# Optimization experiments

Measured on AMD Instinct MI355X. Metric: run time of the kernel, lower is better.

The kernel has to match this reference:

```python
import jax, jax.numpy as jnp
import numpy as np

B, N, D, H = 4, 4096, 1024, 16
DK = D // H  # 64


def setup_inputs() -> dict:
    key = jax.random.key(0)
    ks = jax.random.split(key, 11)
    s_in = 1.0 / np.sqrt(D)
    s_out = 1.0 / np.sqrt(H * DK)
    return {
        "query": jax.random.normal(ks[0], (B, N, D), jnp.float32),
        "key": jax.random.normal(ks[1], (B, N, D), jnp.float32),
        "value": jax.random.normal(ks[2], (B, N, D), jnp.float32),
        # stacked per-head Linear weights (torch Linear: y = x @ W.T + b)
        "Wq": jax.random.uniform(ks[3], (H, DK, D), jnp.float32, -s_in, s_in),
        "bq": jax.random.uniform(ks[4], (H, DK), jnp.float32, -s_in, s_in),
        "Wk": jax.random.uniform(ks[5], (H, DK, D), jnp.float32, -s_in, s_in),
        "bk": jax.random.uniform(ks[6], (H, DK), jnp.float32, -s_in, s_in),
        "Wv": jax.random.uniform(ks[7], (H, DK, D), jnp.float32, -s_in, s_in),
        "bv": jax.random.uniform(ks[8], (H, DK), jnp.float32, -s_in, s_in),
        "Wo": jax.random.uniform(ks[9], (D, H * DK), jnp.float32, -s_out, s_out),
        "bo": jax.random.uniform(ks[10], (D,), jnp.float32, -s_out, s_out),
    }


def reference(query, key, value, Wq, bq, Wk, bk, Wv, bv, Wo, bo):
    b, n, _ = query.shape
    # batched per-head projections: [b,h,n,d_k]
    q = jnp.einsum('bnd,hkd->bhnk', query, Wq) + bq[None, :, None, :]
    k = jnp.einsum('bnd,hkd->bhnk', key, Wk) + bk[None, :, None, :]
    v = jnp.einsum('bnd,hkd->bhnk', value, Wv) + bv[None, :, None, :]
    # linear dot-product attention (faithful: scale by batch**-0.5)
    q = jax.nn.softmax(q, axis=-1) * (b ** -0.5)
    k = jax.nn.softmax(k, axis=-2)  # softmax over sequence dim
    ctx = jnp.einsum('bhnd,bhne->bhde', k, v)      # [b,h,d_k,d_v]
    attn = jnp.einsum('bhnd,bhde->bhne', q, ctx)   # [b,h,n,d_v]
    # concat heads along last dim: [b,n,h*d_v]
    concat = attn.transpose(0, 2, 1, 3).reshape(b, n, -1)
    return concat @ Wo.T + bo
```

## Files before the change

kernel.cpp:

```cpp
#include <hip/hip_runtime.h>
#include <hip/hip_bf16.h>
#include <stdint.h>

#define B_  4
#define N_  4096
#define D_  1024
#define H_  16
#define DK_ 64
#define M_  (B_ * N_)

typedef __attribute__((ext_vector_type(8))) short  short8;
typedef __attribute__((ext_vector_type(4))) float  f32x4;
typedef __attribute__((ext_vector_type(4))) unsigned int u32x4;

__device__ __forceinline__ uint16_t f2bf(float f) {
  union { float f; uint32_t u; } v; v.f = f;
  uint32_t r = v.u + 0x7FFF + ((v.u >> 16) & 1);
  return (uint16_t)(r >> 16);
}
__device__ __forceinline__ uint32_t f2bf2(float lo, float hi) {
  return (uint32_t)f2bf(lo) | ((uint32_t)f2bf(hi) << 16);
}
__device__ __forceinline__ float bf2f(uint16_t u) {
  union { uint32_t u; float f; } v; v.u = ((uint32_t)u) << 16;
  return v.f;
}

__device__ __forceinline__ void gload_lds16(const void* g, void* l) {
  __builtin_amdgcn_global_load_lds((const __attribute__((address_space(1))) void*)g,
                                   (__attribute__((address_space(3))) void*)l, 16, 0, 0);
}

#define S_BARRIER() __builtin_amdgcn_s_barrier()
#define FENCE_LGKM0() asm volatile("s_waitcnt lgkmcnt(0)" ::: "memory")
#define FENCE_VM4()   asm volatile("s_waitcnt vmcnt(4) lgkmcnt(0)" ::: "memory")
#define FENCE_VM0()   asm volatile("s_waitcnt vmcnt(0) lgkmcnt(0)" ::: "memory")

__global__ __launch_bounds__(256) void pack_bf16_kernel(
    const float* q, const float* k, const float* v,
    const float* wq, const float* wk, const float* wv, const float* wo,
    uint16_t* xq, uint16_t* xk, uint16_t* xv,
    uint16_t* bwq, uint16_t* bwk, uint16_t* bwv, uint16_t* bwo)
{
  const float* src; uint16_t* dst; int count;
  switch (blockIdx.y) {
    case 0: src = q;  dst = xq;  count = M_ * D_; break;
    case 1: src = k;  dst = xk;  count = M_ * D_; break;
    case 2: src = v;  dst = xv;  count = M_ * D_; break;
    case 3: src = wq; dst = bwq; count = D_ * D_; break;
    case 4: src = wk; dst = bwk; count = D_ * D_; break;
    case 5: src = wv; dst = bwv; count = D_ * D_; break;
    default: src = wo; dst = bwo; count = D_ * D_; break;
  }
  int base = blockIdx.x * 16384;
  if (base >= count) return;
  int t = threadIdx.x;
#pragma unroll
  for (int it = 0; it < 8; ++it) {
    int idx = base + it * 2048 + t * 8;
    f32x4 f0 = *(const f32x4*)(src + idx);
    f32x4 f1 = *(const f32x4*)(src + idx + 4);
    u32x4 o;
    o.x = f2bf2(f0.x, f0.y); o.y = f2bf2(f0.z, f0.w);
    o.z = f2bf2(f1.x, f1.y); o.w = f2bf2(f1.z, f1.w);
    *(u32x4*)(dst + idx) = o;
  }
}

template<int EPI>
__device__ __forceinline__ void gemm_epilogue(
    f32x4 (&acc)[8][4], int tid, int l, int lr, int kg, int wr, int wc,
    int brow, int bcol, const float* __restrict__ bias, void* __restrict__ C,
    float* __restrict__ pm, float* __restrict__ ps,
    float* sredm, float* sreds)
{
  if (EPI == 2) {
    float bv[4];
#pragma unroll
    for (int ni = 0; ni < 4; ++ni) bv[ni] = bias[bcol * 256 + wc * 64 + ni * 16 + lr];
#pragma unroll
    for (int mi = 0; mi < 8; ++mi) {
#pragma unroll
      for (int j = 0; j < 4; ++j) {
        float v0 = acc[mi][0][j] + bv[0];
        float v1 = acc[mi][1][j] + bv[1];
        float v2 = acc[mi][2][j] + bv[2];
        float v3 = acc[mi][3][j] + bv[3];
        float m = fmaxf(fmaxf(v0, v1), fmaxf(v2, v3));
#pragma unroll
        for (int o = 1; o < 16; o <<= 1) m = fmaxf(m, __shfl_xor(m, o));
        float p0 = __expf(v0 - m), p1 = __expf(v1 - m);
        float p2 = __expf(v2 - m), p3 = __expf(v3 - m);
        float s = (p0 + p1) + (p2 + p3);
#pragma unroll
        for (int o = 1; o < 16; o <<= 1) s += __shfl_xor(s, o);
        float sc = 0.5f / s;
        int row = brow * 256 + wr * 128 + mi * 16 + kg * 4 + j;
        uint16_t* out = (uint16_t*)C + (size_t)row * D_ + bcol * 256 + wc * 64 + lr;
        out[0]  = f2bf(p0 * sc);
        out[16] = f2bf(p1 * sc);
        out[32] = f2bf(p2 * sc);
        out[48] = f2bf(p3 * sc);
      }
    }
  } else if (EPI == 3) {
#pragma unroll
    for (int ni = 0; ni < 4; ++ni) {
      int coll = wc * 64 + ni * 16 + lr;
      int col = bcol * 256 + coll;
      float bvn = bias[col];
      float vals[8][4];
      float m = -1e30f;
#pragma unroll
      for (int mi = 0; mi < 8; ++mi)
#pragma unroll
        for (int j = 0; j < 4; ++j) {
          float val = acc[mi][ni][j] + bvn;
          vals[mi][j] = val;
          m = fmaxf(m, val);
          int row = brow * 256 + wr * 128 + mi * 16 + kg * 4 + j;
          ((uint16_t*)C)[(size_t)row * D_ + col] = f2bf(val);
        }
      m = fmaxf(m, __shfl_xor(m, 16));
      m = fmaxf(m, __shfl_xor(m, 32));
      float s = 0.f;
#pragma unroll
      for (int mi = 0; mi < 8; ++mi)
#pragma unroll
        for (int j = 0; j < 4; ++j) s += __expf(vals[mi][j] - m);
      s += __shfl_xor(s, 16);
      s += __shfl_xor(s, 32);
      if (l < 16) {
        sredm[wr * 256 + coll] = m;
        sreds[wr * 256 + coll] = s;
      }
    }
    __syncthreads();
    if (tid < 256) {
      float m0 = sredm[tid], m1 = sredm[256 + tid];
      float s0 = sreds[tid], s1 = sreds[256 + tid];
      float m = fmaxf(m0, m1);
      float s = s0 * __expf(m0 - m) + s1 * __expf(m1 - m);
      pm[(size_t)brow * D_ + bcol * 256 + tid] = m;
      ps[(size_t)brow * D_ + bcol * 256 + tid] = s;
    }
  } else {
#pragma unroll
    for (int mi = 0; mi < 8; ++mi) {
#pragma unroll
      for (int ni = 0; ni < 4; ++ni) {
        int col = bcol * 256 + wc * 64 + ni * 16 + lr;
        float bv = bias[col];
#pragma unroll
        for (int j = 0; j < 4; ++j) {
          int row = brow * 256 + wr * 128 + mi * 16 + kg * 4 + j;
          float val = acc[mi][ni][j] + bv;
          if (EPI == 1) ((float*)C)[(size_t)row * D_ + col] = val;
          else          ((uint16_t*)C)[(size_t)row * D_ + col] = f2bf(val);
        }
      }
    }
  }
}

__device__ __forceinline__ void gemm256_body(
    const uint16_t* __restrict__ A, const uint16_t* __restrict__ Wb,
    uint16_t* As, uint16_t* Bs,
    int tid, int w, int arow0, int bcrow0, int srcswz, int rsw,
    int lr, int kg, int wr, int wc, f32x4 (&acc)[8][4])
{
  const int NT = 16;
  auto stage_half = [&](const uint16_t* g, int row0, int kt, uint16_t* ldst, int h) {
#pragma unroll
    for (int i = 0; i < 2; ++i) {
      int lin = h * 16384 + i * 8192 + tid * 16;
      int src = lin ^ srcswz;
      const uint16_t* gp = g + (size_t)(row0 + (src >> 7)) * D_ + kt * 64 + ((src & 127) >> 1);
      uint16_t* lp = ldst + h * 8192 + i * 4096 + w * 512;
      gload_lds16(gp, lp);
    }
  };
  auto rdfrag = [&](const uint16_t* tile, int row, int ks) -> short8 {
    return *(const short8*)(tile + row * 64 + ((((ks << 2) | kg) ^ rsw) << 3));
  };

  stage_half(A, arow0, 0, As, 0);  stage_half(A, arow0, 0, As, 1);
  stage_half(Wb, bcrow0, 0, Bs, 0); stage_half(Wb, bcrow0, 0, Bs, 1);
  stage_half(A, arow0, 1, As + 16384, 0); stage_half(A, arow0, 1, As + 16384, 1);
  FENCE_VM4();
  S_BARRIER();

  short8 af0[4][2], af1[4][2], bfr[2][2];
  for (int t = 0; t < NT; ++t) {
    const int p = t & 1;
    uint16_t* Ap = As + p * 16384;
    uint16_t* Bp = Bs + p * 16384;
    uint16_t* Bn = Bs + (p ^ 1) * 16384;

#pragma unroll
    for (int mi = 0; mi < 4; ++mi)
#pragma unroll
      for (int ks = 0; ks < 2; ++ks)
        af0[mi][ks] = rdfrag(Ap, wr * 128 + mi * 16 + lr, ks);
#pragma unroll
    for (int ni = 0; ni < 2; ++ni)
#pragma unroll
      for (int ks = 0; ks < 2; ++ks)
        bfr[ni][ks] = rdfrag(Bp, wc * 64 + ni * 16 + lr, ks);
    if (t + 1 < NT) stage_half(Wb, bcrow0, t + 1, Bn, 0);
    S_BARRIER();
    __builtin_amdgcn_s_setprio(1);
#pragma unroll
    for (int mi = 0; mi < 4; ++mi)
#pragma unroll
      for (int ni = 0; ni < 2; ++ni)
#pragma unroll
        for (int ks = 0; ks < 2; ++ks)
          acc[mi][ni] = __builtin_amdgcn_mfma_f32_16x16x32_bf16(af0[mi][ks], bfr[ni][ks], acc[mi][ni], 0, 0, 0);
    __builtin_amdgcn_s_setprio(0);
    FENCE_LGKM0();
    S_BARRIER();

#pragma unroll
    for (int mi = 0; mi < 4; ++mi)
#pragma unroll
      for (int ks = 0; ks < 2; ++ks)
        af1[mi][ks] = rdfrag(Ap, wr * 128 + 64 + mi * 16 + lr, ks);
    if (t + 1 < NT) stage_half(Wb, bcrow0, t + 1, Bn, 1);
    S_BARRIER();
    __builtin_amdgcn_s_setprio(1);
#pragma unroll
    for (int mi = 0; mi < 4; ++mi)
#pragma unroll
      for (int ni = 0; ni < 2; ++ni)
#pragma unroll
        for (int ks = 0; ks < 2; ++ks)
          acc[mi + 4][ni] = __builtin_amdgcn_mfma_f32_16x16x32_bf16(af1[mi][ks], bfr[ni][ks], acc[mi + 4][ni], 0, 0, 0);
    __builtin_amdgcn_s_setprio(0);
    FENCE_LGKM0();
    S_BARRIER();

#pragma unroll
    for (int ni = 0; ni < 2; ++ni)
#pragma unroll
      for (int ks = 0; ks < 2; ++ks)
        bfr[ni][ks] = rdfrag(Bp, wc * 64 + (ni + 2) * 16 + lr, ks);
    if (t + 2 < NT) stage_half(A, arow0, t + 2, Ap, 0);
    S_BARRIER();
    __builtin_amdgcn_s_setprio(1);
#pragma unroll
    for (int mi = 0; mi < 4; ++mi)
#pragma unroll
      for (int ni = 0; ni < 2; ++ni)
#pragma unroll
        for (int ks = 0; ks < 2; ++ks)
          acc[mi + 4][ni + 2] = __builtin_amdgcn_mfma_f32_16x16x32_bf16(af1[mi][ks], bfr[ni][ks], acc[mi + 4][ni + 2], 0, 0, 0);
    __builtin_amdgcn_s_setprio(0);
    FENCE_LGKM0();
    S_BARRIER();

    if (t + 2 < NT) stage_half(A, arow0, t + 2, Ap, 1);
    S_BARRIER();
    __builtin_amdgcn_s_setprio(1);
#pragma unroll
    for (int mi = 0; mi < 4; ++mi)
#pragma unroll
      for (int ni = 0; ni < 2; ++ni)
#pragma unroll
        for (int ks = 0; ks < 2; ++ks)
          acc[mi][ni + 2] = __builtin_amdgcn_mfma_f32_16x16x32_bf16(af0[mi][ks], bfr[ni][ks], acc[mi][ni + 2], 0, 0, 0);
    __builtin_amdgcn_s_setprio(0);
    if (t <= 13)      { FENCE_VM4(); }
    else if (t == 14) { FENCE_VM0(); }
    else              { FENCE_LGKM0(); }
    S_BARRIER();
  }
}

__global__ __launch_bounds__(512, 2) void qkv_gemm256_kernel(
    const uint16_t* __restrict__ XQ, const uint16_t* __restrict__ XK,
    const uint16_t* __restrict__ XV,
    const uint16_t* __restrict__ WQ, const uint16_t* __restrict__ WK,
    const uint16_t* __restrict__ WV,
    const float* __restrict__ bq, const float* __restrict__ bk,
    const float* __restrict__ bv,
    uint16_t* __restrict__ QS, uint16_t* __restrict__ KP,
    uint16_t* __restrict__ VP,
    float* __restrict__ pm, float* __restrict__ ps)
{
  extern __shared__ uint16_t smem[];
  uint16_t* As = smem;
  uint16_t* Bs = smem + 32768;
  float* sredm = (float*)(smem + 65536);
  float* sreds = sredm + 512;

  const int tid = threadIdx.x;
  const int w = tid >> 6, l = tid & 63;
  const int lr = l & 15, kg = l >> 4;
  const int wr = w >> 2, wc = w & 3;
  const int rsw = lr & 7;
  const int srcswz = ((tid >> 3) & 7) << 4;

  const int flat = blockIdx.y * 4 + blockIdx.x;
  const int swzf = (flat & 7) * 32 + (flat >> 3);
  const int brow = swzf >> 2, bcol = swzf & 3;
  const int z = blockIdx.z;

  const uint16_t* A = (z == 0) ? XQ : (z == 1) ? XK : XV;
  const uint16_t* W = (z == 0) ? WQ : (z == 1) ? WK : WV;
  const float* bias = (z == 0) ? bq : (z == 1) ? bk : bv;
  void* C          = (z == 0) ? (void*)QS : (z == 1) ? (void*)KP : (void*)VP;

  f32x4 acc[8][4];
#pragma unroll
  for (int i = 0; i < 8; ++i)
#pragma unroll
    for (int j = 0; j < 4; ++j) acc[i][j] = (f32x4){0.f, 0.f, 0.f, 0.f};

  gemm256_body(A, W, As, Bs, tid, w, brow * 256, bcol * 256, srcswz, rsw,
               lr, kg, wr, wc, acc);

  if (z == 0)
    gemm_epilogue<2>(acc, tid, l, lr, kg, wr, wc, brow, bcol, bias, C, pm, ps, sredm, sreds);
  else if (z == 1)
    gemm_epilogue<3>(acc, tid, l, lr, kg, wr, wc, brow, bcol, bias, C, pm, ps, sredm, sreds);
  else
    gemm_epilogue<0>(acc, tid, l, lr, kg, wr, wc, brow, bcol, bias, C, pm, ps, sredm, sreds);
}

__global__ __launch_bounds__(512, 2) void gemm256_kernel(
    const uint16_t* __restrict__ A,
    const uint16_t* __restrict__ W,
    const float* __restrict__ bias,
    void* __restrict__ C)
{
  extern __shared__ uint16_t smem[];
  uint16_t* As = smem;
  uint16_t* Bs = smem + 32768;

  const int tid = threadIdx.x;
  const int w = tid >> 6, l = tid & 63;
  const int lr = l & 15, kg = l >> 4;
  const int wr = w >> 2, wc = w & 3;
  const int rsw = lr & 7;
  const int srcswz = ((tid >> 3) & 7) << 4;

  const int flat = blockIdx.y * 4 + blockIdx.x;
  const int swzf = (flat & 7) * 32 + (flat >> 3);
  const int brow = swzf >> 2, bcol = swzf & 3;

  const uint16_t* Wb = W + (size_t)(brow >> 4) * ((size_t)D_ * D_);

  f32x4 acc[8][4];
#pragma unroll
  for (int i = 0; i < 8; ++i)
#pragma unroll
    for (int j = 0; j < 4; ++j) acc[i][j] = (f32x4){0.f, 0.f, 0.f, 0.f};

  gemm256_body(A, Wb, As, Bs, tid, w, brow * 256, bcol * 256, srcswz, rsw,
               lr, kg, wr, wc, acc);

  gemm_epilogue<1>(acc, tid, l, lr, kg, wr, wc, brow, bcol, bias, C,
                   nullptr, nullptr, nullptr, nullptr);
}

__global__ __launch_bounds__(256) void colstats_final_kernel(
    const float* __restrict__ pm, const float* __restrict__ ps,
    float* __restrict__ cmax, float* __restrict__ cinv)
{
  int f = blockIdx.x * 256 + threadIdx.x;
  int b = f >> 10, col = f & 1023;
  float m = -1e30f;
  for (int c = 0; c < 16; ++c) m = fmaxf(m, pm[(size_t)(b * 16 + c) * D_ + col]);
  float s = 0.f;
  for (int c = 0; c < 16; ++c)
    s += ps[(size_t)(b * 16 + c) * D_ + col] * __expf(pm[(size_t)(b * 16 + c) * D_ + col] - m);
  cmax[f] = m;
  cinv[f] = 1.f / s;
}

__global__ __launch_bounds__(256) void ctx_partial_kernel(
    const uint16_t* __restrict__ kp, const uint16_t* __restrict__ vp,
    const float* __restrict__ cmax, const float* __restrict__ cinv,
    float* __restrict__ ctxp)
{
  __shared__ float wk[64][64];
  __shared__ float vt[64][64];
  __shared__ float cm[64], ci[64];
  int t = threadIdx.x;
  int nchunk = blockIdx.x, h = blockIdx.y, b = blockIdx.z;
  if (t < 64) {
    cm[t] = cmax[b * D_ + h * 64 + t];
    ci[t] = cinv[b * D_ + h * 64 + t];
  }
  __syncthreads();
  int d0 = (t >> 4) * 4, e0 = (t & 15) * 4;
  f32x4 acc[4];
#pragma unroll
  for (int i = 0; i < 4; ++i) acc[i] = (f32x4){0.f, 0.f, 0.f, 0.f};

  for (int tt = 0; tt < 8; ++tt) {
    int n0 = nchunk * 512 + tt * 64;
#pragma unroll
    for (int i = 0; i < 4; ++i) {
      int qq = i * 256 + t;
      int r = qq >> 4, c4 = (qq & 15) * 4;
      size_t gi = (size_t)(b * N_ + n0 + r) * D_ + h * 64 + c4;
      union { uint16_t s[4]; uint2 u; } kk, vv;
      kk.u = *(const uint2*)(kp + gi);
      vv.u = *(const uint2*)(vp + gi);
#pragma unroll
      for (int j = 0; j < 4; ++j) {
        wk[r][c4 + j] = __expf(bf2f(kk.s[j]) - cm[c4 + j]) * ci[c4 + j];
        vt[r][c4 + j] = bf2f(vv.s[j]);
      }
    }
    __syncthreads();
#pragma unroll 8
    for (int n = 0; n < 64; ++n) {
      f32x4 wv = *(const f32x4*)&wk[n][d0];
      f32x4 vv4 = *(const f32x4*)&vt[n][e0];
#pragma unroll
      for (int di = 0; di < 4; ++di) acc[di] = acc[di] + vv4 * wv[di];
    }
    __syncthreads();
  }
  float* out = ctxp + (size_t)(nchunk * 64 + b * 16 + h) * 4096;
#pragma unroll
  for (int di = 0; di < 4; ++di)
    *(f32x4*)(out + (d0 + di) * 64 + e0) = acc[di];
}

__global__ __launch_bounds__(256) void ctx_reduce_kernel(
    const float* __restrict__ ctxp, float* __restrict__ ctx)
{
  int o = (blockIdx.x * 256 + threadIdx.x) * 4;
  f32x4 s = (f32x4){0.f, 0.f, 0.f, 0.f};
  for (int c = 0; c < 8; ++c) s = s + *(const f32x4*)(ctxp + (size_t)c * 262144 + o);
  *(f32x4*)(ctx + o) = s;
}

__global__ __launch_bounds__(256) void w2t_kernel(
    const float* __restrict__ ctx,
    const uint16_t* __restrict__ wo,
    uint16_t* __restrict__ w2t)
{
  __shared__ float ctxL[64][65];
  __shared__ float woL[64][65];
  int t = threadIdx.x;
  int otile = blockIdx.x, h = blockIdx.y, b = blockIdx.z;
  const float* csrc = ctx + (size_t)(b * 16 + h) * 4096;
#pragma unroll
  for (int i = 0; i < 4; ++i) {
    int idx = (i * 256 + t) * 4;
    int r = idx >> 6, c = idx & 63;
    f32x4 cv = *(const f32x4*)(csrc + idx);
    union { uint16_t s[4]; uint2 u; } wv;
    wv.u = *(const uint2*)(wo + (size_t)(otile * 64 + r) * D_ + h * 64 + c);
#pragma unroll
    for (int j = 0; j < 4; ++j) {
      ctxL[r][c + j] = cv[j];
      woL[r][c + j] = bf2f(wv.s[j]);
    }
  }
  __syncthreads();
  int ol = (t & 15) * 4, dl = (t >> 4) * 4;
  float acc[4][4];
#pragma unroll
  for (int i = 0; i < 4; ++i)
#pragma unroll
    for (int j = 0; j < 4; ++j) acc[i][j] = 0.f;
#pragma unroll 4
  for (int e = 0; e < 64; ++e) {
    float cv[4], wv[4];
#pragma unroll
    for (int i = 0; i < 4; ++i) { cv[i] = ctxL[dl + i][e]; wv[i] = woL[ol + i][e]; }
#pragma unroll
    for (int di = 0; di < 4; ++di)
#pragma unroll
      for (int oi = 0; oi < 4; ++oi) acc[di][oi] += cv[di] * wv[oi];
  }
  uint16_t* dst = w2t + (size_t)b * D_ * D_ + (size_t)(otile * 64) * D_ + h * 64;
#pragma unroll
  for (int oi = 0; oi < 4; ++oi) {
    union { uint16_t s[4]; uint2 u; } o4;
#pragma unroll
    for (int di = 0; di < 4; ++di) o4.s[di] = f2bf(acc[di][oi]);
    *(uint2*)(dst + (size_t)(ol + oi) * D_ + dl) = o4.u;
  }
}

extern "C" void kernel_launch(void* const* d_in, const int* in_sizes, int n_in,
                              void* d_out, int out_size, void* d_ws, size_t ws_size,
                              hipStream_t stream)
{
  const float* q  = (const float*)d_in[0];
  const float* k  = (const float*)d_in[1];
  const float* v  = (const float*)d_in[2];
  const float* Wq = (const float*)d_in[3];
  const float* bq = (const float*)d_in[4];
  const float* Wk = (const float*)d_in[5];
  const float* bk = (const float*)d_in[6];
  const float* Wv = (const float*)d_in[7];
  const float* bv = (const float*)d_in[8];
  const float* Wo = (const float*)d_in[9];
  const float* bo = (const float*)d_in[10];

  char* ws = (char*)d_ws;
  const size_t XB = (size_t)M_ * D_ * 2;
  const size_t WB = (size_t)D_ * D_ * 2;
  uint16_t* XQ  = (uint16_t*)(ws);
  uint16_t* XK  = (uint16_t*)(ws + XB);
  uint16_t* XV  = (uint16_t*)(ws + 2 * XB);
  uint16_t* WQb = (uint16_t*)(ws + 3 * XB);
  uint16_t* WKb = (uint16_t*)(ws + 3 * XB + WB);
  uint16_t* WVb = (uint16_t*)(ws + 3 * XB + 2 * WB);
  uint16_t* WOb = (uint16_t*)(ws + 3 * XB + 3 * WB);
  uint16_t* QS  = (uint16_t*)(ws + 3 * XB + 4 * WB);
  uint16_t* KP  = (uint16_t*)(ws + 4 * XB + 4 * WB);
  uint16_t* VP  = (uint16_t*)(ws + 5 * XB + 4 * WB);
  float* pm = (float*)d_out;
  float* ps = (float*)((char*)d_out + (256 << 10));
  float* cmax = (float*)XK;
  float* cinv = (float*)((char*)XK + (16 << 10));
  float* ctxp = (float*)((char*)XK + (1 << 20));
  float* ctx  = (float*)((char*)XK + (9 << 20));
  uint16_t* W2T = XQ;

  const size_t LDSB = 135168;

  pack_bf16_kernel<<<dim3(1024, 7), 256, 0, stream>>>(
      q, k, v, Wq, Wk, Wv, Wo, XQ, XK, XV, WQb, WKb, WVb, WOb);

  qkv_gemm256_kernel<<<dim3(4, 64, 3), 512, LDSB, stream>>>(
      XQ, XK, XV, WQb, WKb, WVb, bq, bk, bv, QS, KP, VP, pm, ps);

  colstats_final_kernel<<<16, 256, 0, stream>>>(pm, ps, cmax, cinv);

  ctx_partial_kernel<<<dim3(8, H_, B_), 256, 0, stream>>>(KP, VP, cmax, cinv, ctxp);
  ctx_reduce_kernel<<<256, 256, 0, stream>>>(ctxp, ctx);

  w2t_kernel<<<dim3(16, 16, 4), 256, 0, stream>>>(ctx, WOb, W2T);

  gemm256_kernel<<<dim3(4, 64), 512, LDSB, stream>>>(QS, W2T, bo, d_out);
}
```

Before: 268.9 us.

## Use bf16 MFMA for context accumulation and precompute GEMM staging pointers

The context partial kernel now stages exp-weighted K and V into LDS as transposed bf16 tiles, using cross-lane shuffles to do the transpose, and computes K^T V with 16x16x32 bf16 MFMA instead of scalar fp32 FMAs. Separately, the 256-tile GEMM body precomputes its global source pointers and LDS offsets once, cutting address arithmetic out of the staging calls in the main loop. The MFMA change rounds the softmax weights to bf16, which loses some precision, and the shuffle-based transpose adds lane-exchange work.

```diff
diff --git a/kernel.cpp b/kernel.cpp
--- a/kernel.cpp
+++ b/kernel.cpp
@@ -170,23 +170,35 @@
     int lr, int kg, int wr, int wc, f32x4 (&acc)[8][4])
 {
   const int NT = 16;
-  auto stage_half = [&](const uint16_t* g, int row0, int kt, uint16_t* ldst, int h) {
+  const uint16_t* gA[2][2];
+  const uint16_t* gB[2][2];
+  int lOff[2][2];
+#pragma unroll
+  for (int h = 0; h < 2; ++h)
 #pragma unroll
     for (int i = 0; i < 2; ++i) {
       int lin = h * 16384 + i * 8192 + tid * 16;
       int src = lin ^ srcswz;
-      const uint16_t* gp = g + (size_t)(row0 + (src >> 7)) * D_ + kt * 64 + ((src & 127) >> 1);
-      uint16_t* lp = ldst + h * 8192 + i * 4096 + w * 512;
-      gload_lds16(gp, lp);
-    }
+      size_t rowoff = (size_t)(src >> 7) * D_ + ((src & 127) >> 1);
+      gA[h][i] = A + (size_t)arow0 * D_ + rowoff;
+      gB[h][i] = Wb + (size_t)bcrow0 * D_ + rowoff;
+      lOff[h][i] = h * 8192 + i * 4096 + w * 512;
+    }
+  auto stageA = [&](int kt, uint16_t* ldst, int h) {
+    gload_lds16(gA[h][0] + kt * 64, ldst + lOff[h][0]);
+    gload_lds16(gA[h][1] + kt * 64, ldst + lOff[h][1]);
+  };
+  auto stageB = [&](int kt, uint16_t* ldst, int h) {
+    gload_lds16(gB[h][0] + kt * 64, ldst + lOff[h][0]);
+    gload_lds16(gB[h][1] + kt * 64, ldst + lOff[h][1]);
   };
   auto rdfrag = [&](const uint16_t* tile, int row, int ks) -> short8 {
     return *(const short8*)(tile + row * 64 + ((((ks << 2) | kg) ^ rsw) << 3));
   };
 
-  stage_half(A, arow0, 0, As, 0);  stage_half(A, arow0, 0, As, 1);
-  stage_half(Wb, bcrow0, 0, Bs, 0); stage_half(Wb, bcrow0, 0, Bs, 1);
-  stage_half(A, arow0, 1, As + 16384, 0); stage_half(A, arow0, 1, As + 16384, 1);
+  stageA(0, As, 0); stageA(0, As, 1);
+  stageB(0, Bs, 0); stageB(0, Bs, 1);
+  stageA(1, As + 16384, 0); stageA(1, As + 16384, 1);
   FENCE_VM4();
   S_BARRIER();
 
@@ -207,7 +219,7 @@
 #pragma unroll
       for (int ks = 0; ks < 2; ++ks)
         bfr[ni][ks] = rdfrag(Bp, wc * 64 + ni * 16 + lr, ks);
-    if (t + 1 < NT) stage_half(Wb, bcrow0, t + 1, Bn, 0);
+    if (t + 1 < NT) stageB(t + 1, Bn, 0);
     S_BARRIER();
     __builtin_amdgcn_s_setprio(1);
 #pragma unroll
@@ -226,7 +238,7 @@
 #pragma unroll
       for (int ks = 0; ks < 2; ++ks)
         af1[mi][ks] = rdfrag(Ap, wr * 128 + 64 + mi * 16 + lr, ks);
-    if (t + 1 < NT) stage_half(Wb, bcrow0, t + 1, Bn, 1);
+    if (t + 1 < NT) stageB(t + 1, Bn, 1);
     S_BARRIER();
     __builtin_amdgcn_s_setprio(1);
 #pragma unroll
@@ -245,7 +257,7 @@
 #pragma unroll
       for (int ks = 0; ks < 2; ++ks)
         bfr[ni][ks] = rdfrag(Bp, wc * 64 + (ni + 2) * 16 + lr, ks);
-    if (t + 2 < NT) stage_half(A, arow0, t + 2, Ap, 0);
+    if (t + 2 < NT) stageA(t + 2, Ap, 0);
     S_BARRIER();
     __builtin_amdgcn_s_setprio(1);
 #pragma unroll
@@ -259,7 +271,7 @@
     FENCE_LGKM0();
     S_BARRIER();
 
-    if (t + 2 < NT) stage_half(A, arow0, t + 2, Ap, 1);
+    if (t + 2 < NT) stageA(t + 2, Ap, 1);
     S_BARRIER();
     __builtin_amdgcn_s_setprio(1);
 #pragma unroll
@@ -384,17 +396,19 @@
     const float* __restrict__ cmax, const float* __restrict__ cinv,
     float* __restrict__ ctxp)
 {
-  __shared__ float wk[64][64];
-  __shared__ float vt[64][64];
+  __shared__ uint16_t wt[64][72];
+  __shared__ uint16_t vt[64][72];
   __shared__ float cm[64], ci[64];
-  int t = threadIdx.x;
-  int nchunk = blockIdx.x, h = blockIdx.y, b = blockIdx.z;
+  const int t = threadIdx.x;
+  const int w = t >> 6, l = t & 63;
+  const int lr = l & 15, p = l >> 4;
+  const int nchunk = blockIdx.x, h = blockIdx.y, b = blockIdx.z;
   if (t < 64) {
     cm[t] = cmax[b * D_ + h * 64 + t];
     ci[t] = cinv[b * D_ + h * 64 + t];
   }
   __syncthreads();
-  int d0 = (t >> 4) * 4, e0 = (t & 15) * 4;
+
   f32x4 acc[4];
 #pragma unroll
   for (int i = 0; i < 4; ++i) acc[i] = (f32x4){0.f, 0.f, 0.f, 0.f};
@@ -403,32 +417,59 @@
     int n0 = nchunk * 512 + tt * 64;
 #pragma unroll
     for (int i = 0; i < 4; ++i) {
-      int qq = i * 256 + t;
-      int r = qq >> 4, c4 = (qq & 15) * 4;
+      int r = i * 16 + w * 4 + p;
+      int c4 = lr * 4;
       size_t gi = (size_t)(b * N_ + n0 + r) * D_ + h * 64 + c4;
       union { uint16_t s[4]; uint2 u; } kk, vv;
       kk.u = *(const uint2*)(kp + gi);
       vv.u = *(const uint2*)(vp + gi);
-#pragma unroll
-      for (int j = 0; j < 4; ++j) {
-        wk[r][c4 + j] = __expf(bf2f(kk.s[j]) - cm[c4 + j]) * ci[c4 + j];
-        vt[r][c4 + j] = bf2f(vv.s[j]);
+      float a0 = __expf(bf2f(kk.s[0]) - cm[c4 + 0]) * ci[c4 + 0];
+      float a1 = __expf(bf2f(kk.s[1]) - cm[c4 + 1]) * ci[c4 + 1];
+      float a2 = __expf(bf2f(kk.s[2]) - cm[c4 + 2]) * ci[c4 + 2];
+      float a3 = __expf(bf2f(kk.s[3]) - cm[c4 + 3]) * ci[c4 + 3];
+      float s0 = __shfl_xor(a0, 16), s1 = __shfl_xor(a1, 16);
+      float s2 = __shfl_xor(a2, 16), s3 = __shfl_xor(a3, 16);
+      float c0 = (p & 1) ? s1 : a0, c1 = (p & 1) ? a1 : s0;
+      float c2 = (p & 1) ? s3 : a2, c3 = (p & 1) ? a3 : s2;
+      float S0 = __shfl_xor(c0, 32), S1 = __shfl_xor(c1, 32);
+      float S2 = __shfl_xor(c2, 32), S3 = __shfl_xor(c3, 32);
+      float e0 = (p & 2) ? S2 : c0, e1 = (p & 2) ? S3 : c1;
+      float e2 = (p & 2) ? c2 : S0, e3 = (p & 2) ? c3 : S1;
+      int rbase = i * 16 + w * 4;
+      int cc = lr * 4 + p;
+      *(uint2*)&wt[cc][rbase] = make_uint2(f2bf2(e0, e1), f2bf2(e2, e3));
+      int b0 = vv.s[0], b1 = vv.s[1], b2 = vv.s[2], b3 = vv.s[3];
+      int t0 = __shfl_xor(b0, 16), t1 = __shfl_xor(b1, 16);
+      int t2 = __shfl_xor(b2, 16), t3 = __shfl_xor(b3, 16);
+      int d0 = (p & 1) ? t1 : b0, d1 = (p & 1) ? b1 : t0;
+      int d2 = (p & 1) ? t3 : b2, d3 = (p & 1) ? b3 : t2;
+      int T0 = __shfl_xor(d0, 32), T1 = __shfl_xor(d1, 32);
+      int T2 = __shfl_xor(d2, 32), T3 = __shfl_xor(d3, 32);
+      uint32_t f0 = (p & 2) ? T2 : d0, f1 = (p & 2) ? T3 : d1;
+      uint32_t f2v = (p & 2) ? d2 : T0, f3 = (p & 2) ? d3 : T1;
+      *(uint2*)&vt[cc][rbase] =
+          make_uint2((f0 & 0xFFFFu) | (f1 << 16), (f2v & 0xFFFFu) | (f3 << 16));
+    }
+    __syncthreads();
+    short8 af[2];
+#pragma unroll
+    for (int ks = 0; ks < 2; ++ks)
+      af[ks] = *(const short8*)(&wt[w * 16 + lr][ks * 32 + p * 8]);
+#pragma unroll
+    for (int ni = 0; ni < 4; ++ni)
+#pragma unroll
+      for (int ks = 0; ks < 2; ++ks) {
+        short8 bfv = *(const short8*)(&vt[ni * 16 + lr][ks * 32 + p * 8]);
+        acc[ni] = __builtin_amdgcn_mfma_f32_16x16x32_bf16(af[ks], bfv, acc[ni], 0, 0, 0);
       }
-    }
     __syncthreads();
-#pragma unroll 8
-    for (int n = 0; n < 64; ++n) {
-      f32x4 wv = *(const f32x4*)&wk[n][d0];
-      f32x4 vv4 = *(const f32x4*)&vt[n][e0];
-#pragma unroll
-      for (int di = 0; di < 4; ++di) acc[di] = acc[di] + vv4 * wv[di];
-    }
-    __syncthreads();
   }
   float* out = ctxp + (size_t)(nchunk * 64 + b * 16 + h) * 4096;
 #pragma unroll
-  for (int di = 0; di < 4; ++di)
-    *(f32x4*)(out + (d0 + di) * 64 + e0) = acc[di];
+  for (int ni = 0; ni < 4; ++ni)
+#pragma unroll
+    for (int j = 0; j < 4; ++j)
+      out[(w * 16 + p * 4 + j) * 64 + ni * 16 + lr] = acc[ni][j];
 }
 
 __global__ __launch_bounds__(256) void ctx_reduce_kernel(
```

Result: faster. 261.8 us (-2.7%).
